# Optimization experiments

Hardware: AMD Instinct MI355X
Metric: run time of the kernel (lower is better)

Reference implementation:

```python
import jax, jax.numpy as jnp
import numpy as np

N_NODES = 16384      # original graph nodes (rows of incidence matrix H)
E = 131072           # line-graph nodes = original edges
M = 2097152          # line-graph edges (avg degree 16)
IN = 64              # input feature dim
HEADS = 4
CH = 64              # per-head channels (concat=False -> output dim = CH)


def setup_inputs() -> dict:
    key = jax.random.key(0)
    ks = jax.random.split(key, 8)
    x = jax.random.normal(ks[0], (E, IN), jnp.float32)
    edge_index = jax.random.randint(ks[1], (2, M), 0, E)
    rows = jax.random.randint(ks[2], (E,), 0, N_NODES)
    W = jax.random.normal(ks[3], (HEADS * CH, IN), jnp.float32) * 0.05
    att_src = jax.random.normal(ks[4], (HEADS, CH), jnp.float32) * 0.05
    att_dst = jax.random.normal(ks[5], (HEADS, CH), jnp.float32) * 0.05
    bias = jnp.zeros((CH,), jnp.float32)
    w_weight = jax.random.normal(ks[6], (CH, CH), jnp.float32) * 0.05
    w_bias = jnp.zeros((CH,), jnp.float32)
    return dict(x=x, edge_index=edge_index, rows=rows, W=W, att_src=att_src,
                att_dst=att_dst, bias=bias, w_weight=w_weight, w_bias=w_bias,
                n_nodes=N_NODES)


def reference(x, edge_index, rows, W, att_src, att_dst, bias, w_weight, w_bias, n_nodes):
    e_nodes = x.shape[0]
    heads, ch = att_src.shape
    # GATConv linear projection: [E, heads, ch]
    h = (x @ W.T).reshape(e_nodes, heads, ch)
    a_src = jnp.einsum('ehc,hc->eh', h, att_src)
    a_dst = jnp.einsum('ehc,hc->eh', h, att_dst)
    # PyG GATConv adds self-loops by default
    self_loop = jnp.arange(e_nodes)
    src = jnp.concatenate([edge_index[0], self_loop])
    dst = jnp.concatenate([edge_index[1], self_loop])
    # edge attention logits + segment softmax over incoming edges per dst
    logits = jax.nn.leaky_relu(a_src[src] + a_dst[dst], 0.2)   # [Mtot, heads]
    lmax = jax.ops.segment_max(logits, dst, num_segments=e_nodes)
    ex = jnp.exp(logits - lmax[dst])
    denom = jax.ops.segment_sum(ex, dst, num_segments=e_nodes)
    alpha = ex / (denom[dst] + 1e-16)
    # weighted scatter aggregation
    msg = h[src] * alpha[:, :, None]                            # [Mtot, heads, ch]
    out = jax.ops.segment_sum(msg, dst, num_segments=e_nodes)
    out = out.mean(axis=1) + bias                               # concat=False -> mean heads
    # incidence-matrix normalization D @ H @ x == scatter-mean of edge feats to nodes
    agg = jax.ops.segment_sum(out, rows, num_segments=n_nodes)
    deg = jax.ops.segment_sum(jnp.ones((e_nodes,), out.dtype), rows, num_segments=n_nodes)
    agg = jnp.where(deg[:, None] > 0, agg / jnp.maximum(deg, 1.0)[:, None], 0.0)
    return agg @ w_weight.T + w_bias
```

## Files before the change

kernel.cpp:

```cpp
#include <hip/hip_runtime.h>
#include <hip/hip_bf16.h>


#define CAP 64
#define NBKT 256
#define CELLCAP 24
#define NFILL 2048
#define QST 196

using frag16 = __attribute__((ext_vector_type(8))) short;
using f32x4  = __attribute__((ext_vector_type(4))) float;
using f32x2  = __attribute__((ext_vector_type(2))) float;

__device__ __forceinline__ unsigned short f2bf(float f) {
  union { float f; unsigned u; } v; v.f = f;
  return (unsigned short)((v.u + 0x8000u) >> 16);
}
__device__ __forceinline__ float bflo(unsigned u) {
  union { unsigned u; float f; } v; v.u = u << 16; return v.f;
}
__device__ __forceinline__ float bfhi(unsigned u) {
  union { unsigned u; float f; } v; v.u = u & 0xffff0000u; return v.f;
}
__device__ __forceinline__ unsigned pkbf(float lo, float hi) {
  union { __hip_bfloat162 b; unsigned u; } v;
  v.b = __float22bfloat162_rn(make_float2(lo, hi));
  return v.u;
}

__global__ __launch_bounds__(256) void k_prevs(
    const float* __restrict__ W, const float* __restrict__ att_src,
    const float* __restrict__ att_dst, unsigned short* __restrict__ Btr,
    float* __restrict__ vs) {
  int t = blockIdx.x * 256 + threadIdx.x;
  {
    int c = t >> 8, kap = t & 255;
    int h = kap >> 6, k = kap & 63;
    Btr[t] = f2bf(0.25f * W[(size_t)(h * 64 + c) * 64 + k]);
  }
  if (blockIdx.x < 2) {
    int o = blockIdx.x * 256 + threadIdx.x;
    int j = o >> 6, c = o & 63;
    const float* att = (j < 4) ? att_src : att_dst;
    int hh = j & 3;
    float s = 0.f;
    for (int ch = 0; ch < 64; ++ch)
      s += W[(size_t)(hh * 64 + ch) * 64 + c] * att[hh * 64 + ch];
    vs[o] = s;
  }
}

__device__ __forceinline__ void adot_body(
    const float* __restrict__ x, const float* __restrict__ vs,
    unsigned short* __restrict__ xb,
    float* __restrict__ a_src, float* __restrict__ a_dst, int bid,
    float* vsl) {
  const int t = threadIdx.x;
  if (t < 128) ((float4*)vsl)[t] = ((const float4*)vs)[t];
  __syncthreads();
  const int w = t >> 6, lane = t & 63, l15 = lane & 15, l4 = lane >> 4;
  const int row = bid * 64 + w * 16 + l15;

  const float4* xp = (const float4*)(x + (size_t)row * 64 + l4 * 16);
  float4 v0 = xp[0], v1 = xp[1], v2 = xp[2], v3 = xp[3];
  float xa[16] = {v0.x, v0.y, v0.z, v0.w, v1.x, v1.y, v1.z, v1.w,
                  v2.x, v2.y, v2.z, v2.w, v3.x, v3.y, v3.z, v3.w};

  uint2* dst = (uint2*)(xb + (size_t)row * 64 + l4 * 16);
  dst[0] = make_uint2(pkbf(xa[0], xa[1]),   pkbf(xa[2], xa[3]));
  dst[1] = make_uint2(pkbf(xa[4], xa[5]),   pkbf(xa[6], xa[7]));
  dst[2] = make_uint2(pkbf(xa[8], xa[9]),   pkbf(xa[10], xa[11]));
  dst[3] = make_uint2(pkbf(xa[12], xa[13]), pkbf(xa[14], xa[15]));

  float pj[8];
#pragma unroll
  for (int j = 0; j < 8; ++j) {
    const float4* q = (const float4*)(vsl + j * 64 + l4 * 16);
    float4 q0 = q[0], q1 = q[1], q2 = q[2], q3 = q[3];
    float s = xa[0] * q0.x + xa[1] * q0.y + xa[2] * q0.z + xa[3] * q0.w
            + xa[4] * q1.x + xa[5] * q1.y + xa[6] * q1.z + xa[7] * q1.w
            + xa[8] * q2.x + xa[9] * q2.y + xa[10] * q2.z + xa[11] * q2.w
            + xa[12] * q3.x + xa[13] * q3.y + xa[14] * q3.z + xa[15] * q3.w;
    s += __shfl_xor(s, 16, 64);
    s += __shfl_xor(s, 32, 64);
    pj[j] = s;
  }
  if (l4 == 0) {
    *(float4*)&a_src[(size_t)row * 4] = make_float4(pj[0], pj[1], pj[2], pj[3]);
    *(float4*)&a_dst[(size_t)row * 4] = make_float4(pj[4], pj[5], pj[6], pj[7]);
  }
}

__device__ __forceinline__ void fill1_body(
    const int* __restrict__ ei, int M,
    int* __restrict__ buf, unsigned short* __restrict__ cntbb, int bid,
    int* bcnt ) {
  const int t = threadIdx.x;
  bcnt[t] = 0;
  __syncthreads();
  const int base = bid * 1024 + t;
  int ss[4], dd[4];
#pragma unroll
  for (int i = 0; i < 4; ++i) {
    int m = base + i * 256;
    ss[i] = ei[m];
    dd[i] = ei[M + m];
  }
#pragma unroll
  for (int i = 0; i < 4; ++i) {
    int b = dd[i] >> 9;
    int slot = atomicAdd(&bcnt[b], 1);
    if (slot < CELLCAP)
      buf[((size_t)b * NFILL + bid) * CELLCAP + slot] =
          (ss[i] << 9) | (dd[i] & 511);
  }
  __syncthreads();
  int c = bcnt[t];
  cntbb[(size_t)t * NFILL + bid] = (unsigned short)(c < CELLCAP ? c : CELLCAP);
}

__global__ __launch_bounds__(256, 8) void k_fused(
    const float* __restrict__ x, const float* __restrict__ vs,
    unsigned short* __restrict__ xb,
    float* __restrict__ a_src, float* __restrict__ a_dst,
    const int* __restrict__ ei, int M, int E,
    int* __restrict__ buf, unsigned short* __restrict__ cntbb,
    int ncast, int nfill) {
  __shared__ float vsl[512];
  __shared__ int bcnt[NBKT];
  const int bid = blockIdx.x;
  int npair = 2 * min(ncast, nfill);
  if (bid < npair) {
    if (bid & 1) adot_body(x, vs, xb, a_src, a_dst, bid >> 1, vsl);
    else         fill1_body(ei, M, buf, cntbb, bid >> 1, bcnt);
  } else {
    int r = bid - npair;
    if (nfill > ncast) fill1_body(ei, M, buf, cntbb, ncast + r, bcnt);
    else               adot_body(x, vs, xb, a_src, a_dst, ncast + r, vsl);
  }
}

__global__ __launch_bounds__(256) void k_fill2(
    const int* __restrict__ buf, const unsigned short* __restrict__ cntbb,
    int* __restrict__ cnt, int* __restrict__ csr) {
  __shared__ int c2[512];
  const int b = blockIdx.x, t = threadIdx.x;
  c2[t] = 1; c2[t + 256] = 1;
  csr[((size_t)(b * 512 + t)) * CAP] = b * 512 + t;
  csr[((size_t)(b * 512 + 256 + t)) * CAP] = b * 512 + 256 + t;
  __syncthreads();
  for (int cell = t; cell < NFILL; cell += 256) {
    int c = cntbb[(size_t)b * NFILL + cell];
    const int4* cp = (const int4*)(buf + ((size_t)b * NFILL + cell) * CELLCAP);
    int4 r0 = cp[0], r1 = cp[1], r2 = cp[2], r3 = cp[3], r4 = cp[4], r5 = cp[5];
#define STEP(J, V) if ((J) < c) { \
      int pk = (V); int dl = pk & 511, s = pk >> 9; \
      int pos = atomicAdd(&c2[dl], 1); \
      if (pos < CAP) csr[((size_t)(b * 512 + dl)) * CAP + pos] = s; }
    STEP(0, r0.x)  STEP(1, r0.y)  STEP(2, r0.z)  STEP(3, r0.w)
    STEP(4, r1.x)  STEP(5, r1.y)  STEP(6, r1.z)  STEP(7, r1.w)
    STEP(8, r2.x)  STEP(9, r2.y)  STEP(10, r2.z) STEP(11, r2.w)
    STEP(12, r3.x) STEP(13, r3.y) STEP(14, r3.z) STEP(15, r3.w)
    STEP(16, r4.x) STEP(17, r4.y) STEP(18, r4.z) STEP(19, r4.w)
    STEP(20, r5.x) STEP(21, r5.y) STEP(22, r5.z) STEP(23, r5.w)
#undef STEP
  }
  __syncthreads();
  cnt[b * 512 + t] = c2[t];
  cnt[b * 512 + 256 + t] = c2[t + 256];
}

__global__ __launch_bounds__(256) void k_agg(
    const unsigned short* __restrict__ xb, const float4* __restrict__ a_src,
    const float4* __restrict__ a_dst, const int* __restrict__ cnt,
    const int* __restrict__ csr, const int* __restrict__ rows,
    const unsigned short* __restrict__ Btr, const float* __restrict__ bias,
    float* __restrict__ agg, int* __restrict__ degc, int E) {
  __shared__ unsigned shm[16 * QST];
  const int w = threadIdx.x >> 6, lane = threadIdx.x & 63;
  const int q = lane >> 4, d4 = lane & 15;
  const int li = w * 4 + q;
  const int e = blockIdx.x * 16 + li;
  const int base = li * QST;

  int deg = cnt[e];
  if (deg > CAP) deg = CAP;
  float4 ad = a_dst[e];

  float exs[4][4];
  int   srcs[4];
  float s0 = 0.f, s1 = 0.f, s2 = 0.f, s3 = 0.f;
#pragma unroll
  for (int s = 0; s < 4; ++s) {
    int k = d4 + s * 16;
    float e0 = 0.f, e1 = 0.f, e2 = 0.f, e3 = 0.f;
    int sk = 0;
    if (k < deg) {
      sk = csr[(size_t)e * CAP + k];
      float4 as = a_src[sk];
      float l0 = as.x + ad.x; l0 = l0 > 0.f ? l0 : 0.2f * l0;
      float l1 = as.y + ad.y; l1 = l1 > 0.f ? l1 : 0.2f * l1;
      float l2 = as.z + ad.z; l2 = l2 > 0.f ? l2 : 0.2f * l2;
      float l3 = as.w + ad.w; l3 = l3 > 0.f ? l3 : 0.2f * l3;
      e0 = __expf(l0); e1 = __expf(l1); e2 = __expf(l2); e3 = __expf(l3);
    }
    srcs[s] = sk;
    exs[s][0] = e0; exs[s][1] = e1; exs[s][2] = e2; exs[s][3] = e3;
    s0 += e0; s1 += e1; s2 += e2; s3 += e3;
  }
#pragma unroll
  for (int off = 8; off > 0; off >>= 1) {
    s0 += __shfl_xor(s0, off, 64);
    s1 += __shfl_xor(s1, off, 64);
    s2 += __shfl_xor(s2, off, 64);
    s3 += __shfl_xor(s3, off, 64);
  }
  float i0 = 1.f / (s0 + 1e-16f), i1 = 1.f / (s1 + 1e-16f);
  float i2 = 1.f / (s2 + 1e-16f), i3 = 1.f / (s3 + 1e-16f);

#pragma unroll
  for (int s = 0; s < 4; ++s) {
    int k = d4 + s * 16;
    if (k < deg) {
      *(uint2*)&shm[base + 2 * k] =
          make_uint2(pkbf(exs[s][0] * i0, exs[s][1] * i1),
                     pkbf(exs[s][2] * i2, exs[s][3] * i3));
      shm[base + 128 + k] = (unsigned)(srcs[s] << 7);
    }
  }

  const char* xrow = (const char*)xb + d4 * 8;

#define LD(K) (*(const uint2*)(xrow + (size_t)shm[base + 128 + (K)]))
#define CONS(K, V) { \
    uint2 A_ = *(const uint2*)&shm[base + 2 * (K)]; \
    f32x2 xa_; xa_.x = bflo((V).x); xa_.y = bfhi((V).x); \
    f32x2 xb_; xb_.x = bflo((V).y); xb_.y = bfhi((V).y); \
    float a0_ = bflo(A_.x), a1_ = bfhi(A_.x); \
    float a2_ = bflo(A_.y), a3_ = bfhi(A_.y); \
    f32x2 c0_ = {a0_, a0_}, c1_ = {a1_, a1_}; \
    f32x2 c2_ = {a2_, a2_}, c3_ = {a3_, a3_}; \
    z0a += c0_ * xa_; z0b += c0_ * xb_; \
    z1a += c1_ * xa_; z1b += c1_ * xb_; \
    z2a += c2_ * xa_; z2b += c2_ * xb_; \
    z3a += c3_ * xa_; z3b += c3_ * xb_; }

  f32x2 z0a = {0.f, 0.f}, z0b = {0.f, 0.f}, z1a = {0.f, 0.f}, z1b = {0.f, 0.f};
  f32x2 z2a = {0.f, 0.f}, z2b = {0.f, 0.f}, z3a = {0.f, 0.f}, z3b = {0.f, 0.f};
  int k = 0;
  if (deg >= 4) {
    uint2 v0 = LD(0), v1 = LD(1), v2 = LD(2), v3 = LD(3);
    for (; k + 8 <= deg; k += 4) {
      uint2 n0 = LD(k + 4), n1 = LD(k + 5), n2 = LD(k + 6), n3 = LD(k + 7);
      CONS(k, v0) CONS(k + 1, v1) CONS(k + 2, v2) CONS(k + 3, v3)
      v0 = n0; v1 = n1; v2 = n2; v3 = n3;
    }
    CONS(k, v0) CONS(k + 1, v1) CONS(k + 2, v2) CONS(k + 3, v3)
    k += 4;
  }
  for (; k < deg; ++k) {
    uint2 v = LD(k);
    CONS(k, v)
  }
#undef LD
#undef CONS

  {
    unsigned short* zw = (unsigned short*)&shm[base] + 4 * d4;
    *(uint2*)&zw[0 * 64] = make_uint2(pkbf(z0a.x, z0a.y), pkbf(z0b.x, z0b.y));
    *(uint2*)&zw[1 * 64] = make_uint2(pkbf(z1a.x, z1a.y), pkbf(z1b.x, z1b.y));
    *(uint2*)&zw[2 * 64] = make_uint2(pkbf(z2a.x, z2a.y), pkbf(z2b.x, z2b.y));
    *(uint2*)&zw[3 * 64] = make_uint2(pkbf(z3a.x, z3a.y), pkbf(z3b.x, z3b.y));
  }
  __syncthreads();

  const int l15 = lane & 15, l4 = lane >> 4;
  const unsigned short* bp = Btr + (size_t)(w * 16 + l15) * 256 + l4 * 8;
  const unsigned short* zp = (const unsigned short*)&shm[l15 * QST] + l4 * 8;
  f32x4 acc = {0.f, 0.f, 0.f, 0.f};
#pragma unroll
  for (int kk = 0; kk < 8; ++kk) {
    frag16 af  = *(const frag16*)(zp + kk * 32);
    frag16 bfg = *(const frag16*)(bp + kk * 32);
    acc = __builtin_amdgcn_mfma_f32_16x16x32_bf16(af, bfg, acc, 0, 0, 0);
  }
  {
    int ccol = w * 16 + l15;
    float bs = bias[ccol];
#pragma unroll
    for (int r = 0; r < 4; ++r) {
      int ee = blockIdx.x * 16 + l4 * 4 + r;
      atomicAdd(&agg[(size_t)rows[ee] * 64 + ccol], acc[r] + bs);
    }
  }
  if (d4 == 0) atomicAdd(&degc[rows[e]], 1);
}

__global__ __launch_bounds__(256) void k_final(
    const float* __restrict__ agg, const int* __restrict__ degc,
    const float* __restrict__ wgt, const float* __restrict__ wb,
    float* __restrict__ out, int N) {
  __shared__ float wtt[64 * 65];
  const int t = threadIdx.x;
#pragma unroll
  for (int i = 0; i < 16; ++i) {
    int idx = t + i * 256;
    wtt[(idx & 63) * 65 + (idx >> 6)] = wgt[idx];
  }
  __syncthreads();
  const int w = t >> 6, lane = t & 63;
  int n = blockIdx.x * 4 + w;
  if (n >= N) return;
  int dg = degc[n];
  float av = dg > 0 ? agg[(size_t)n * 64 + lane] / (float)dg : 0.f;
  float o = 0.f;
#pragma unroll
  for (int k = 0; k < 64; ++k) {
    o += __shfl(av, k, 64) * wtt[k * 65 + lane];
  }
  out[(size_t)n * 64 + lane] = o + wb[lane];
}

extern "C" void kernel_launch(void* const* d_in, const int* in_sizes, int n_in,
                              void* d_out, int out_size, void* d_ws, size_t ws_size,
                              hipStream_t stream) {
  const float* x       = (const float*)d_in[0];
  const int*   ei      = (const int*)d_in[1];
  const int*   rows    = (const int*)d_in[2];
  const float* W       = (const float*)d_in[3];
  const float* att_src = (const float*)d_in[4];
  const float* att_dst = (const float*)d_in[5];
  const float* bias    = (const float*)d_in[6];
  const float* wgt     = (const float*)d_in[7];
  const float* wb      = (const float*)d_in[8];

  const int E = in_sizes[0] / 64;
  const int M = in_sizes[1] / 2;
  const int N = out_size / 64;

  char* p = (char*)d_ws;
  int*   buf   = (int*)p;                   p += (size_t)NBKT * NFILL * CELLCAP * 4;
  unsigned short* cntbb = (unsigned short*)p; p += (size_t)NBKT * NFILL * 2;
  int*   csr   = (int*)p;                   p += (size_t)E * CAP * 4;
  unsigned short* xb = (unsigned short*)p;  p += (size_t)E * 64 * 2;
  float* a_src = (float*)p;                 p += (size_t)E * 4 * 4;
  float* a_dst = (float*)p;                 p += (size_t)E * 4 * 4;
  int*   cnt   = (int*)p;                   p += (size_t)E * 4;
  float* agg   = (float*)p;                 p += (size_t)N * 64 * 4;
  int*   degc  = (int*)p;                   p += (size_t)N * 4;
  unsigned short* Btr = (unsigned short*)p; p += 64 * 256 * 2;
  float* vs    = (float*)p;                 p += 512 * 4;

  hipMemsetAsync(agg, 0, (size_t)N * 64 * 4 + (size_t)N * 4, stream);

  k_prevs<<<64, 256, 0, stream>>>(W, att_src, att_dst, Btr, vs);

  const int ncast = E / 64;
  const int nfill = NFILL;
  k_fused<<<ncast + nfill, 256, 0, stream>>>(
      x, vs, xb, a_src, a_dst, ei, M, E, buf, cntbb, ncast, nfill);

  k_fill2<<<NBKT, 256, 0, stream>>>(buf, cntbb, cnt, csr);

  k_agg<<<E / 16, 256, 0, stream>>>(
      xb, (const float4*)a_src, (const float4*)a_dst, cnt, csr,
      rows, Btr, bias, agg, degc, E);

  k_final<<<(N + 3) / 4, 256, 0, stream>>>(agg, degc, wgt, wb, (float*)d_out, N);
}
```

Baseline: 170.3 us.

## Stage bucket cells in LDS, pack counts into entries, read only used slots

The first fill pass now stages each block's bucketed edges in shared memory and writes each bucket cell as six full int4 stores, with the cell count packed into the high bits of the first entry. The layout is transposed to block-major order and the separate count array is removed. The second pass reads the count from the first int4, always reads the first two int4s, and loads further int4s only when the count requires them, which cuts scattered writes and unused reads. In exchange it uses 24KB of extra LDS per block, lowers launch bounds occupancy from 8 to 4, and masks the source index bits in the first entry (17 bits), which assumes E fits in 17 bits.

```diff
diff --git a/kernel.cpp b/kernel.cpp
--- a/kernel.cpp
+++ b/kernel.cpp
@@ -93,8 +93,8 @@
 
 __device__ __forceinline__ void fill1_body(
     const int* __restrict__ ei, int M,
-    int* __restrict__ buf, unsigned short* __restrict__ cntbb, int bid,
-    int* bcnt ) {
+    int* __restrict__ buf, int bid,
+    int* bcnt , int* stage ) {
   const int t = threadIdx.x;
   bcnt[t] = 0;
   __syncthreads();
@@ -111,38 +111,48 @@
     int b = dd[i] >> 9;
     int slot = atomicAdd(&bcnt[b], 1);
     if (slot < CELLCAP)
-      buf[((size_t)b * NFILL + bid) * CELLCAP + slot] =
-          (ss[i] << 9) | (dd[i] & 511);
+      stage[b * CELLCAP + slot] = (ss[i] << 9) | (dd[i] & 511);
   }
   __syncthreads();
   int c = bcnt[t];
-  cntbb[(size_t)t * NFILL + bid] = (unsigned short)(c < CELLCAP ? c : CELLCAP);
-}
-
-__global__ __launch_bounds__(256, 8) void k_fused(
+  if (c > CELLCAP) c = CELLCAP;
+  int e0 = (c > 0 ? stage[t * CELLCAP] : 0) | (c << 26);
+  int4* dst = (int4*)(buf + ((size_t)bid * NBKT + t) * CELLCAP);
+  const int4* sp = (const int4*)(stage + t * CELLCAP);
+  int4 r0 = sp[0];
+  r0.x = e0;
+  dst[0] = r0;
+  dst[1] = sp[1];
+  dst[2] = sp[2];
+  dst[3] = sp[3];
+  dst[4] = sp[4];
+  dst[5] = sp[5];
+}
+
+__global__ __launch_bounds__(256, 4) void k_fused(
     const float* __restrict__ x, const float* __restrict__ vs,
     unsigned short* __restrict__ xb,
     float* __restrict__ a_src, float* __restrict__ a_dst,
     const int* __restrict__ ei, int M, int E,
-    int* __restrict__ buf, unsigned short* __restrict__ cntbb,
-    int ncast, int nfill) {
+    int* __restrict__ buf, int ncast, int nfill) {
   __shared__ float vsl[512];
   __shared__ int bcnt[NBKT];
+  __shared__ int stage[NBKT * CELLCAP];
   const int bid = blockIdx.x;
   int npair = 2 * min(ncast, nfill);
   if (bid < npair) {
     if (bid & 1) adot_body(x, vs, xb, a_src, a_dst, bid >> 1, vsl);
-    else         fill1_body(ei, M, buf, cntbb, bid >> 1, bcnt);
+    else         fill1_body(ei, M, buf, bid >> 1, bcnt, stage);
   } else {
     int r = bid - npair;
-    if (nfill > ncast) fill1_body(ei, M, buf, cntbb, ncast + r, bcnt);
+    if (nfill > ncast) fill1_body(ei, M, buf, ncast + r, bcnt, stage);
     else               adot_body(x, vs, xb, a_src, a_dst, ncast + r, vsl);
   }
 }
 
 __global__ __launch_bounds__(256) void k_fill2(
-    const int* __restrict__ buf, const unsigned short* __restrict__ cntbb,
-    int* __restrict__ cnt, int* __restrict__ csr) {
+    const int* __restrict__ buf, int* __restrict__ cnt,
+    int* __restrict__ csr) {
   __shared__ int c2[512];
   const int b = blockIdx.x, t = threadIdx.x;
   c2[t] = 1; c2[t + 256] = 1;
@@ -150,19 +160,23 @@
   csr[((size_t)(b * 512 + 256 + t)) * CAP] = b * 512 + 256 + t;
   __syncthreads();
   for (int cell = t; cell < NFILL; cell += 256) {
-    int c = cntbb[(size_t)b * NFILL + cell];
-    const int4* cp = (const int4*)(buf + ((size_t)b * NFILL + cell) * CELLCAP);
-    int4 r0 = cp[0], r1 = cp[1], r2 = cp[2], r3 = cp[3], r4 = cp[4], r5 = cp[5];
-#define STEP(J, V) if ((J) < c) { \
-      int pk = (V); int dl = pk & 511, s = pk >> 9; \
+    const int4* cp = (const int4*)(buf + ((size_t)cell * NBKT + b) * CELLCAP);
+    int4 r0 = cp[0], r1 = cp[1];
+    int c = (r0.x >> 26) & 63;
+#define STEP(J, V, MASK) if ((J) < c) { \
+      int pk = (V); int dl = pk & 511; \
+      int s = (pk >> 9) & (MASK); \
       int pos = atomicAdd(&c2[dl], 1); \
       if (pos < CAP) csr[((size_t)(b * 512 + dl)) * CAP + pos] = s; }
-    STEP(0, r0.x)  STEP(1, r0.y)  STEP(2, r0.z)  STEP(3, r0.w)
-    STEP(4, r1.x)  STEP(5, r1.y)  STEP(6, r1.z)  STEP(7, r1.w)
-    STEP(8, r2.x)  STEP(9, r2.y)  STEP(10, r2.z) STEP(11, r2.w)
-    STEP(12, r3.x) STEP(13, r3.y) STEP(14, r3.z) STEP(15, r3.w)
-    STEP(16, r4.x) STEP(17, r4.y) STEP(18, r4.z) STEP(19, r4.w)
-    STEP(20, r5.x) STEP(21, r5.y) STEP(22, r5.z) STEP(23, r5.w)
+    STEP(0, r0.x, 0x1FFFF) STEP(1, r0.y, 0x7FFFFF) STEP(2, r0.z, 0x7FFFFF)
+    STEP(3, r0.w, 0x7FFFFF)
+    STEP(4, r1.x, 0x7FFFFF) STEP(5, r1.y, 0x7FFFFF) STEP(6, r1.z, 0x7FFFFF)
+    STEP(7, r1.w, 0x7FFFFF)
+    for (int j = 8; j < c; j += 4) {
+      int4 r = cp[j >> 2];
+      STEP(j + 0, r.x, 0x7FFFFF) STEP(j + 1, r.y, 0x7FFFFF)
+      STEP(j + 2, r.z, 0x7FFFFF) STEP(j + 3, r.w, 0x7FFFFF)
+    }
 #undef STEP
   }
   __syncthreads();
@@ -340,7 +354,6 @@
 
   char* p = (char*)d_ws;
   int*   buf   = (int*)p;                   p += (size_t)NBKT * NFILL * CELLCAP * 4;
-  unsigned short* cntbb = (unsigned short*)p; p += (size_t)NBKT * NFILL * 2;
   int*   csr   = (int*)p;                   p += (size_t)E * CAP * 4;
   unsigned short* xb = (unsigned short*)p;  p += (size_t)E * 64 * 2;
   float* a_src = (float*)p;                 p += (size_t)E * 4 * 4;
@@ -358,9 +371,9 @@
   const int ncast = E / 64;
   const int nfill = NFILL;
   k_fused<<<ncast + nfill, 256, 0, stream>>>(
-      x, vs, xb, a_src, a_dst, ei, M, E, buf, cntbb, ncast, nfill);
-
-  k_fill2<<<NBKT, 256, 0, stream>>>(buf, cntbb, cnt, csr);
+      x, vs, xb, a_src, a_dst, ei, M, E, buf, ncast, nfill);
+
+  k_fill2<<<NBKT, 256, 0, stream>>>(buf, cnt, csr);
 
   k_agg<<<E / 16, 256, 0, stream>>>(
       xb, (const float4*)a_src, (const float4*)a_dst, cnt, csr,
```

Measured after the change: 180.7 us. 6.1% more time.
